# Kernel optimization log

Measured on AMD Instinct MI355X. Metric: run time of the kernel, lower is better.

## Reference

```python
import jax, jax.numpy as jnp
import numpy as np

B, S, D_MODEL = 4, 4096, 2048
D_SPACE = 128
N_C, N_QK, N_V = 512, 512, 512
TOPK_C, TOPK_QK, TOPK_V = 8, 4, 6


def setup_inputs() -> dict:
    key = jax.random.key(0)
    k1, k2, k3, k4 = jax.random.split(key, 4)
    x = jax.random.normal(k1, (B, S, D_MODEL), dtype=jnp.float32)
    importance = jax.random.uniform(k2, (B, S), dtype=jnp.float32)
    proj_w = jax.random.normal(k3, (D_SPACE, D_MODEL), dtype=jnp.float32) * (1.0 / np.sqrt(D_MODEL))
    proj_b = jnp.zeros((D_SPACE,), dtype=jnp.float32)
    neuron_emb = jax.random.normal(k4, (N_C + N_QK + N_V, D_SPACE), dtype=jnp.float32) * 0.02
    return {"x": x, "importance": importance, "proj_w": proj_w, "proj_b": proj_b, "neuron_emb": neuron_emb}


def _topk_sparsify(w, k):
    # torch: topk -> scatter into zeros -> renormalize
    vals, idx = jax.lax.top_k(w, k)                      # [B,k]
    b = jnp.arange(w.shape[0])[:, None]
    sparse = jnp.zeros_like(w).at[b, idx].set(vals)      # [B,n]
    return sparse / (sparse.sum(axis=-1, keepdims=True) + 1e-8)


def reference(x, importance, proj_w, proj_b, neuron_emb):
    # eval mode: dropout off, no starvation bonus, no EMA / aux loss
    h = jnp.einsum("bsd,ed->bse", x, proj_w) + proj_b          # [B,S,d_space]
    nrm = jnp.linalg.norm(neuron_emb, axis=-1, keepdims=True)
    emb_n = neuron_emb / jnp.maximum(nrm, 1e-12)               # F.normalize
    logits = jnp.einsum("bse,ne->bsn", h, emb_n)               # [B,S,total]

    log_c = logits[..., :N_C]
    log_qk = logits[..., N_C:N_C + N_QK]                        # expand_Q == expand_K slice
    log_v = logits[..., N_C + N_QK:]

    pref_c = jax.nn.softmax(log_c, axis=-1)
    pref_qk = jax.nn.softmax(log_qk, axis=-1)
    pref_v = jax.nn.softmax(log_v, axis=-1)

    dense_c = jnp.einsum("bs,bsn->bn", importance, pref_c)
    dense_qk = jnp.einsum("bs,bsn->bn", importance, pref_qk)
    dense_v = jnp.einsum("bs,bsn->bn", importance, pref_v)

    cw = _topk_sparsify(dense_c, TOPK_C)
    qw = _topk_sparsify(dense_qk, TOPK_QK)   # Q and K use identical logits in eval
    kw = _topk_sparsify(dense_qk, TOPK_QK)
    vw = _topk_sparsify(dense_v, TOPK_V)
    return jnp.stack([cw, qw, kw, vw])       # [4, B, 512]
```

## Files before the change

kernel.cpp:

```cpp
#include <hip/hip_runtime.h>
#include <hip/hip_bf16.h>

#define BATCH 4
#define S_TOT 4096
#define ROWS (BATCH * S_TOT)
#define DM 2048
#define DSP 128
#define NSEG 512

typedef short short8 __attribute__((ext_vector_type(8)));
typedef float f32x16 __attribute__((ext_vector_type(16)));

static __device__ inline short f2bf(float v, float& back) {
  unsigned u = __float_as_uint(v);
  unsigned r = u + 0x7FFFu + ((u >> 16) & 1u);
  unsigned short hs = (unsigned short)(r >> 16);
  back = __uint_as_float(((unsigned)hs) << 16);
  return (short)hs;
}

#define GLL16(gsrc, ldst)                                                       \
  __builtin_amdgcn_global_load_lds(                                             \
      (const __attribute__((address_space(1))) void*)(gsrc),                    \
      (__attribute__((address_space(3))) void*)(ldst), 16, 0, 0)


__global__ __launch_bounds__(64) void k0_prep(const float* __restrict__ W,
                                              const float* __restrict__ emb,
                                              short* __restrict__ wHi,
                                              short* __restrict__ wLo,
                                              short* __restrict__ eHi,
                                              short* __restrict__ eLo) {
  const int l = threadIdx.x;
  if (blockIdx.x < 512) {
    const int tc = blockIdx.x;
    const int t = tc >> 7, c = tc & 127;
    const int n = t * 32 + (l & 31);
    const int k = c * 16 + (l >> 5) * 8;
    const float4 a0 = *(const float4*)&W[(size_t)n * DM + k];
    const float4 a1 = *(const float4*)&W[(size_t)n * DM + k + 4];
    const float av[8] = {a0.x, a0.y, a0.z, a0.w, a1.x, a1.y, a1.z, a1.w};
    short8 hi8, lo8; float bk;
    #pragma unroll
    for (int e = 0; e < 8; ++e) {
      hi8[e] = f2bf(av[e], bk); lo8[e] = f2bf(av[e] - bk, bk);
    }
    const size_t idx = (size_t)tc * 64 + l;
    ((short8*)wHi)[idx] = hi8;
    ((short8*)wLo)[idx] = lo8;
  } else {
    const int row = blockIdx.x - 512;
    __shared__ short sh[128], sl[128];
    float2 v = *(const float2*)&emb[row * 128 + l * 2];
    float ss = v.x * v.x + v.y * v.y;
    #pragma unroll
    for (int m = 32; m; m >>= 1) ss += __shfl_xor(ss, m);
    const float inv = 1.0f / fmaxf(sqrtf(ss), 1e-12f);
    float bk;
    const float ox = v.x * inv, oy = v.y * inv;
    sh[2 * l] = f2bf(ox, bk);     sl[2 * l] = f2bf(ox - bk, bk);
    sh[2 * l + 1] = f2bf(oy, bk); sl[2 * l + 1] = f2bf(oy - bk, bk);
    __syncthreads();
    if (l < 32) {
      const int split = l >> 4, kc = (l >> 1) & 7, kh = l & 1;
      const short* src = (split ? sl : sh) + kc * 16 + kh * 8;
      const short8 val = *(const short8*)src;
      const size_t idx = (size_t)(row >> 5) * 4096 + kc * 512 +
                         ((row & 31) + 32 * kh) * 8;
      *(short8*)((split ? eLo : eHi) + idx) = val;
    }
  }
}

__global__ __launch_bounds__(512, 4) void k1_fused(const float* __restrict__ x,
                                                   const short* __restrict__ wHi,
                                                   const short* __restrict__ wLo,
                                                   const float* __restrict__ bias,
                                                   short* __restrict__ hHi,
                                                   short* __restrict__ hLo) {
  __shared__ __align__(16) float As[2][32][128];
  __shared__ __align__(16) float hsum[32][132];
  __shared__ float bsh[128];
  const int t = threadIdx.x;
  const int wave = t >> 6, lane = t & 63;
  const int fr = lane & 31, ks = lane >> 5;
  const int kh = wave >> 2, wc = wave & 3;
  const int m0 = blockIdx.x * 32;

  if (t < 128) bsh[t] = bias[t];

  const int r0 = 4 * wave + ks;
  const int r1 = r0 + 2;
  const float* xsrc0 = x + (size_t)(m0 + r0) * DM + ((fr ^ (r0 & 7)) << 2);
  const float* xsrc1 = x + (size_t)(m0 + r1) * DM + ((fr ^ (r1 & 7)) << 2);
  float* AsF = &As[0][0][0];
  float* dst0 = AsF + wave * 512;
  float* dst1 = dst0 + 256;

  const short8* bhBase = (const short8*)wHi + (size_t)(wc * 128) * 64 + lane;
  const short8* blBase = (const short8*)wLo + (size_t)(wc * 128) * 64 + lane;
  const int fr7 = fr & 7;

  f32x16 acc = {};

  GLL16(xsrc0, dst0);
  GLL16(xsrc1, dst1);
  __syncthreads();

  #pragma unroll 2
  for (int step = 0; step < 16; ++step) {
    const int buf = step & 1;
    if (step + 1 < 16) {
      GLL16(xsrc0 + (step + 1) * 128, AsF + (buf ^ 1) * 4096 + wave * 512);
      GLL16(xsrc1 + (step + 1) * 128, AsF + (buf ^ 1) * 4096 + wave * 512 + 256);
    }
    const float* abase = AsF + buf * 4096 + fr * 128;
    #pragma unroll
    for (int c = 0; c < 4; ++c) {
      const int g0 = kh * 16 + c * 4 + ks * 2;
      const float4 a0 = *(const float4*)(abase + ((g0 ^ fr7) << 2));
      const float4 a1 = *(const float4*)(abase + (((g0 + 1) ^ fr7) << 2));
      const float av[8] = {a0.x, a0.y, a0.z, a0.w, a1.x, a1.y, a1.z, a1.w};
      short8 ah, al; float bk;
      #pragma unroll
      for (int e = 0; e < 8; ++e) {
        ah[e] = f2bf(av[e], bk); al[e] = f2bf(av[e] - bk, bk);
      }
      const int kcg = step * 8 + kh * 4 + c;
      const short8 bh = bhBase[(size_t)kcg * 64];
      const short8 bl = blBase[(size_t)kcg * 64];
      acc = __builtin_amdgcn_mfma_f32_32x32x16_bf16(ah, bh, acc, 0, 0, 0);
      acc = __builtin_amdgcn_mfma_f32_32x32x16_bf16(ah, bl, acc, 0, 0, 0);
      acc = __builtin_amdgcn_mfma_f32_32x32x16_bf16(al, bh, acc, 0, 0, 0);
    }
    __syncthreads();
  }

  if (kh == 0) {
    #pragma unroll
    for (int reg = 0; reg < 16; ++reg) {
      const int row = (reg & 3) + 8 * (reg >> 2) + 4 * ks;
      hsum[row][wc * 32 + fr] = acc[reg];
    }
  }
  __syncthreads();
  if (kh == 1) {
    #pragma unroll
    for (int reg = 0; reg < 16; ++reg) {
      const int row = (reg & 3) + 8 * (reg >> 2) + 4 * ks;
      hsum[row][wc * 32 + fr] += acc[reg];
    }
  }
  __syncthreads();

  {
    const int row = t >> 4, kc8 = t & 15;
    float v[8];
    #pragma unroll
    for (int j = 0; j < 8; ++j)
      v[j] = hsum[row][kc8 * 8 + j] + bsh[kc8 * 8 + j];
    short8 hi8, lo8; float bk;
    #pragma unroll
    for (int e = 0; e < 8; ++e) {
      hi8[e] = f2bf(v[e], bk); lo8[e] = f2bf(v[e] - bk, bk);
    }
    const int kc = kc8 >> 1, kh2 = kc8 & 1;
    const size_t idx = (size_t)blockIdx.x * 512 + kc * 64 + (row + 32 * kh2);
    ((short8*)hHi)[idx] = hi8;
    ((short8*)hLo)[idx] = lo8;
  }
}

__global__ __launch_bounds__(512, 2) void k2_mfma(const short* __restrict__ hHi,
                                                  const short* __restrict__ hLo,
                                                  const short* __restrict__ eHi,
                                                  const short* __restrict__ eLo,
                                                  const float* __restrict__ imp,
                                                  float* __restrict__ partials) {
  const int t = threadIdx.x;
  const int m0 = blockIdx.x * 64;
  const int seg = blockIdx.y;
  const int wave = t >> 6, lane = t & 63;
  const int wr = wave >> 2;
  const int wc = wave & 3;
  const int fr = lane & 31;
  const int hi = lane >> 5;

  __shared__ float redA[2][32][4];
  __shared__ float redB[2][32][4];
  __shared__ float ldsD[2][512];

  f32x16 acc[4] = {};

  const short8* pAh = (const short8*)hHi + ((m0 >> 5) + wr) * 512 + lane;
  const short8* pAl = (const short8*)hLo + ((m0 >> 5) + wr) * 512 + lane;
  const short8* pBh = (const short8*)eHi + (seg * 16 + wc * 4) * 512 + lane;
  const short8* pBl = (const short8*)eLo + (seg * 16 + wc * 4) * 512 + lane;

  #pragma unroll
  for (int kc = 0; kc < 8; ++kc) {
    const short8 ah = pAh[kc * 64];
    const short8 al = pAl[kc * 64];
    #pragma unroll
    for (int t2 = 0; t2 < 4; ++t2) {
      const short8 bh = pBh[t2 * 512 + kc * 64];
      const short8 bl = pBl[t2 * 512 + kc * 64];
      acc[t2] = __builtin_amdgcn_mfma_f32_32x32x16_bf16(ah, bh, acc[t2], 0, 0, 0);
      acc[t2] = __builtin_amdgcn_mfma_f32_32x32x16_bf16(ah, bl, acc[t2], 0, 0, 0);
      acc[t2] = __builtin_amdgcn_mfma_f32_32x32x16_bf16(al, bh, acc[t2], 0, 0, 0);
    }
  }

  float mx[16];
  #pragma unroll
  for (int r = 0; r < 16; ++r) {
    float m = fmaxf(fmaxf(acc[0][r], acc[1][r]), fmaxf(acc[2][r], acc[3][r]));
    #pragma unroll
    for (int k = 1; k < 32; k <<= 1) m = fmaxf(m, __shfl_xor(m, k));
    mx[r] = m;
  }
  if (fr == 0) {
    #pragma unroll
    for (int r = 0; r < 16; ++r)
      redA[wr][(r & 3) + 8 * (r >> 2) + 4 * hi][wc] = mx[r];
  }
  __syncthreads();
  float M[16];
  #pragma unroll
  for (int r = 0; r < 16; ++r) {
    const int row = (r & 3) + 8 * (r >> 2) + 4 * hi;
    M[r] = fmaxf(fmaxf(redA[wr][row][0], redA[wr][row][1]),
                 fmaxf(redA[wr][row][2], redA[wr][row][3]));
  }

  float sm[16];
  #pragma unroll
  for (int r = 0; r < 16; ++r) {
    float s = 0.0f;
    #pragma unroll
    for (int t2 = 0; t2 < 4; ++t2) {
      const float p = __expf(acc[t2][r] - M[r]);
      acc[t2][r] = p;
      s += p;
    }
    #pragma unroll
    for (int k = 1; k < 32; k <<= 1) s += __shfl_xor(s, k);
    sm[r] = s;
  }
  if (fr == 0) {
    #pragma unroll
    for (int r = 0; r < 16; ++r)
      redB[wr][(r & 3) + 8 * (r >> 2) + 4 * hi][wc] = sm[r];
  }
  __syncthreads();
  float w[16];
  #pragma unroll
  for (int r = 0; r < 16; ++r) {
    const int row = (r & 3) + 8 * (r >> 2) + 4 * hi;
    const float S = (redB[wr][row][0] + redB[wr][row][1]) +
                    (redB[wr][row][2] + redB[wr][row][3]);
    w[r] = imp[m0 + wr * 32 + row] / S;
  }

  #pragma unroll
  for (int t2 = 0; t2 < 4; ++t2) {
    float d = 0.0f;
    #pragma unroll
    for (int r = 0; r < 16; ++r) d = fmaf(acc[t2][r], w[r], d);
    d += __shfl_xor(d, 32);
    if (hi == 0) ldsD[wr][wc * 128 + t2 * 32 + fr] = d;
  }
  __syncthreads();
  partials[((size_t)seg * 256 + blockIdx.x) * 512 + t] = ldsD[0][t] + ldsD[1][t];
}

__global__ __launch_bounds__(256) void k3_topk(const float* __restrict__ partials,
                                               float* __restrict__ out) {
  const int b = blockIdx.x;
  const int seg = blockIdx.y;
  const int tid = threadIdx.x;
  const int K = (seg == 0) ? 8 : ((seg == 1) ? 4 : 6);

  __shared__ float v[512];
  __shared__ float wv[8];
  __shared__ int wi[8];
  __shared__ float redv[4];
  __shared__ int redi[4];

  const float* src = partials + ((size_t)seg * 256 + b * 64) * 512;
  float a0 = 0.f, a1 = 0.f, a2 = 0.f, a3 = 0.f;
  float b0 = 0.f, b1 = 0.f, b2 = 0.f, b3 = 0.f;
  for (int j = 0; j < 64; j += 4) {
    a0 += src[(size_t)(j + 0) * 512 + tid];
    a1 += src[(size_t)(j + 1) * 512 + tid];
    a2 += src[(size_t)(j + 2) * 512 + tid];
    a3 += src[(size_t)(j + 3) * 512 + tid];
    b0 += src[(size_t)(j + 0) * 512 + tid + 256];
    b1 += src[(size_t)(j + 1) * 512 + tid + 256];
    b2 += src[(size_t)(j + 2) * 512 + tid + 256];
    b3 += src[(size_t)(j + 3) * 512 + tid + 256];
  }
  v[tid] = (a0 + a1) + (a2 + a3);
  v[tid + 256] = (b0 + b1) + (b2 + b3);
  __syncthreads();

  for (int t = 0; t < K; ++t) {
    const float v0 = v[tid], v1 = v[tid + 256];
    float bv; int bi;
    if (v1 > v0) { bv = v1; bi = tid + 256; } else { bv = v0; bi = tid; }
    #pragma unroll
    for (int m = 1; m < 64; m <<= 1) {
      const float ov = __shfl_xor(bv, m);
      const int oi = __shfl_xor(bi, m);
      if (ov > bv || (ov == bv && oi < bi)) { bv = ov; bi = oi; }
    }
    if ((tid & 63) == 0) { redv[tid >> 6] = bv; redi[tid >> 6] = bi; }
    __syncthreads();
    if (tid == 0) {
      float best = redv[0]; int besti = redi[0];
      for (int q = 1; q < 4; ++q)
        if (redv[q] > best || (redv[q] == best && redi[q] < besti)) {
          best = redv[q]; besti = redi[q];
        }
      wv[t] = best; wi[t] = besti;
      v[besti] = -3.0e38f;
    }
    __syncthreads();
  }

  float s = 1e-8f;
  for (int t = 0; t < K; ++t) s += wv[t];

  const int slot0 = (seg == 0) ? 0 : ((seg == 1) ? 1 : 3);
  float* o0 = out + slot0 * (BATCH * NSEG) + b * NSEG;
  o0[tid] = 0.0f; o0[tid + 256] = 0.0f;
  float* o1 = nullptr;
  if (seg == 1) {
    o1 = out + 2 * (BATCH * NSEG) + b * NSEG;
    o1[tid] = 0.0f; o1[tid + 256] = 0.0f;
  }
  __syncthreads();
  if (tid < K) {
    const float val = wv[tid] / s;
    o0[wi[tid]] = val;
    if (seg == 1) o1[wi[tid]] = val;
  }
}

extern "C" void kernel_launch(void* const* d_in, const int* in_sizes, int n_in,
                              void* d_out, int out_size, void* d_ws, size_t ws_size,
                              hipStream_t stream) {
  (void)in_sizes; (void)n_in; (void)out_size; (void)ws_size;
  const float* x    = (const float*)d_in[0];
  const float* imp  = (const float*)d_in[1];
  const float* W    = (const float*)d_in[2];
  const float* bias = (const float*)d_in[3];
  const float* emb  = (const float*)d_in[4];
  float* out = (float*)d_out;

  float* partials = (float*)d_ws;
  short* hHi      = (short*)(partials + 768 * 512);
  short* hLo      = hHi + 2097152;
  short* eHi      = hLo + 2097152;
  short* eLo      = eHi + 196608;
  short* wHi      = eLo + 196608;
  short* wLo      = wHi + 262144;

  k0_prep<<<512 + 1536, 64, 0, stream>>>(W, emb, wHi, wLo, eHi, eLo);
  k1_fused<<<ROWS / 32, 512, 0, stream>>>(x, wHi, wLo, bias, hHi, hLo);
  k2_mfma<<<dim3(ROWS / 64, 3), 512, 0, stream>>>(hHi, hLo, eHi, eLo, imp, partials);
  k3_topk<<<dim3(BATCH, 3), 256, 0, stream>>>(partials, out);
}
```

Measured before the change: 113.1 us.

## Double k1 row tile to 64, drop split-K reduction, use packed bf16 convert

```diff
diff --git a/kernel.cpp b/kernel.cpp
--- a/kernel.cpp
+++ b/kernel.cpp
@@ -17,6 +17,25 @@
   unsigned short hs = (unsigned short)(r >> 16);
   back = __uint_as_float(((unsigned)hs) << 16);
   return (short)hs;
+}
+
+static __device__ inline unsigned cvtpk2(float a, float b) {
+  unsigned r;
+  asm("v_cvt_pk_bf16_f32 %0, %1, %2" : "=v"(r) : "v"(a), "v"(b));
+  return r;
+}
+static __device__ inline void cvt8(const float* v, short8& hi8, short8& lo8) {
+  union { short8 s; unsigned u[4]; } H, L;
+  #pragma unroll
+  for (int w = 0; w < 4; ++w) {
+    const float f0 = v[2 * w], f1 = v[2 * w + 1];
+    const unsigned u = cvtpk2(f0, f1);
+    const float b0 = __uint_as_float(u << 16);
+    const float b1 = __uint_as_float(u & 0xffff0000u);
+    L.u[w] = cvtpk2(f0 - b0, f1 - b1);
+    H.u[w] = u;
+  }
+  hi8 = H.s; lo8 = L.s;
 }
 
 #define GLL16(gsrc, ldst)                                                       \
@@ -72,100 +91,88 @@
   }
 }
 
-__global__ __launch_bounds__(512, 4) void k1_fused(const float* __restrict__ x,
+__global__ __launch_bounds__(512, 2) void k1_fused(const float* __restrict__ x,
                                                    const short* __restrict__ wHi,
                                                    const short* __restrict__ wLo,
                                                    const float* __restrict__ bias,
                                                    short* __restrict__ hHi,
                                                    short* __restrict__ hLo) {
-  __shared__ __align__(16) float As[2][32][128];
-  __shared__ __align__(16) float hsum[32][132];
+  __shared__ __align__(16) float As[2][64][128];
   __shared__ float bsh[128];
   const int t = threadIdx.x;
   const int wave = t >> 6, lane = t & 63;
   const int fr = lane & 31, ks = lane >> 5;
-  const int kh = wave >> 2, wc = wave & 3;
-  const int m0 = blockIdx.x * 32;
+  const int rg = wave >> 2, wc = wave & 3;
+  const int m0 = blockIdx.x * 64;
 
   if (t < 128) bsh[t] = bias[t];
 
-  const int r0 = 4 * wave + ks;
-  const int r1 = r0 + 2;
-  const float* xsrc0 = x + (size_t)(m0 + r0) * DM + ((fr ^ (r0 & 7)) << 2);
-  const float* xsrc1 = x + (size_t)(m0 + r1) * DM + ((fr ^ (r1 & 7)) << 2);
+  const float* xs[4];
+  #pragma unroll
+  for (int j = 0; j < 4; ++j) {
+    const int r = 8 * wave + 2 * j + ks;
+    xs[j] = x + (size_t)(m0 + r) * DM + ((fr ^ (2 * j + ks)) << 2);
+  }
   float* AsF = &As[0][0][0];
-  float* dst0 = AsF + wave * 512;
-  float* dst1 = dst0 + 256;
-
-  const short8* bhBase = (const short8*)wHi + (size_t)(wc * 128) * 64 + lane;
-  const short8* blBase = (const short8*)wLo + (size_t)(wc * 128) * 64 + lane;
-  const int fr7 = fr & 7;
+
+  const short8* bhB = (const short8*)wHi + (size_t)(wc * 128) * 64 + lane;
+  const short8* blB = (const short8*)wLo + (size_t)(wc * 128) * 64 + lane;
 
   f32x16 acc = {};
 
-  GLL16(xsrc0, dst0);
-  GLL16(xsrc1, dst1);
-  __syncthreads();
-
-  #pragma unroll 2
+  #define STAGE(buf, step)                                                      \
+    _Pragma("unroll")                                                           \
+    for (int j = 0; j < 4; ++j)                                                 \
+      GLL16(xs[j] + (step) * 128, AsF + (buf) * 8192 + (8 * wave + 2 * j) * 128);
+
+  STAGE(0, 0);
+  __syncthreads();
+
+  #pragma unroll 1
   for (int step = 0; step < 16; ++step) {
     const int buf = step & 1;
-    if (step + 1 < 16) {
-      GLL16(xsrc0 + (step + 1) * 128, AsF + (buf ^ 1) * 4096 + wave * 512);
-      GLL16(xsrc1 + (step + 1) * 128, AsF + (buf ^ 1) * 4096 + wave * 512 + 256);
-    }
-    const float* abase = AsF + buf * 4096 + fr * 128;
-    #pragma unroll
-    for (int c = 0; c < 4; ++c) {
-      const int g0 = kh * 16 + c * 4 + ks * 2;
-      const float4 a0 = *(const float4*)(abase + ((g0 ^ fr7) << 2));
-      const float4 a1 = *(const float4*)(abase + (((g0 + 1) ^ fr7) << 2));
+    if (step + 1 < 16) STAGE(buf ^ 1, step + 1);
+    const float* abase = AsF + buf * 8192 + (rg * 32 + fr) * 128;
+    const int s7 = fr & 7;
+    #pragma unroll
+    for (int c = 0; c < 8; ++c) {
+      const int g0 = c * 4 + ks * 2;
+      const float4 a0 = *(const float4*)(abase + ((g0 ^ s7) << 2));
+      const float4 a1 = *(const float4*)(abase + (((g0 + 1) ^ s7) << 2));
       const float av[8] = {a0.x, a0.y, a0.z, a0.w, a1.x, a1.y, a1.z, a1.w};
-      short8 ah, al; float bk;
-      #pragma unroll
-      for (int e = 0; e < 8; ++e) {
-        ah[e] = f2bf(av[e], bk); al[e] = f2bf(av[e] - bk, bk);
-      }
-      const int kcg = step * 8 + kh * 4 + c;
-      const short8 bh = bhBase[(size_t)kcg * 64];
-      const short8 bl = blBase[(size_t)kcg * 64];
+      short8 ah, al;
+      cvt8(av, ah, al);
+      const int kc = step * 8 + c;
+      const short8 bh = bhB[(size_t)kc * 64];
+      const short8 bl = blB[(size_t)kc * 64];
       acc = __builtin_amdgcn_mfma_f32_32x32x16_bf16(ah, bh, acc, 0, 0, 0);
       acc = __builtin_amdgcn_mfma_f32_32x32x16_bf16(ah, bl, acc, 0, 0, 0);
       acc = __builtin_amdgcn_mfma_f32_32x32x16_bf16(al, bh, acc, 0, 0, 0);
     }
     __syncthreads();
   }
-
-  if (kh == 0) {
-    #pragma unroll
-    for (int reg = 0; reg < 16; ++reg) {
-      const int row = (reg & 3) + 8 * (reg >> 2) + 4 * ks;
-      hsum[row][wc * 32 + fr] = acc[reg];
-    }
-  }
-  __syncthreads();
-  if (kh == 1) {
-    #pragma unroll
-    for (int reg = 0; reg < 16; ++reg) {
-      const int row = (reg & 3) + 8 * (reg >> 2) + 4 * ks;
-      hsum[row][wc * 32 + fr] += acc[reg];
-    }
-  }
-  __syncthreads();
-
-  {
-    const int row = t >> 4, kc8 = t & 15;
+  #undef STAGE
+
+  float* hsum = AsF;
+  #pragma unroll
+  for (int reg = 0; reg < 16; ++reg) {
+    const int row = (reg & 3) + 8 * (reg >> 2) + 4 * ks;
+    hsum[(rg * 32 + row) * 132 + wc * 32 + fr] = acc[reg];
+  }
+  __syncthreads();
+  #pragma unroll
+  for (int i = 0; i < 2; ++i) {
+    const int task = t + 512 * i;
+    const int row = task >> 4, kc8 = task & 15;
     float v[8];
     #pragma unroll
     for (int j = 0; j < 8; ++j)
-      v[j] = hsum[row][kc8 * 8 + j] + bsh[kc8 * 8 + j];
-    short8 hi8, lo8; float bk;
-    #pragma unroll
-    for (int e = 0; e < 8; ++e) {
-      hi8[e] = f2bf(v[e], bk); lo8[e] = f2bf(v[e] - bk, bk);
-    }
+      v[j] = hsum[row * 132 + kc8 * 8 + j] + bsh[kc8 * 8 + j];
+    short8 hi8, lo8;
+    cvt8(v, hi8, lo8);
     const int kc = kc8 >> 1, kh2 = kc8 & 1;
-    const size_t idx = (size_t)blockIdx.x * 512 + kc * 64 + (row + 32 * kh2);
+    const size_t idx = ((size_t)blockIdx.x * 2 + (row >> 5)) * 512 + kc * 64 +
+                       ((row & 31) + 32 * kh2);
     ((short8*)hHi)[idx] = hi8;
     ((short8*)hLo)[idx] = lo8;
   }
@@ -367,7 +374,7 @@
   short* wLo      = wHi + 262144;
 
   k0_prep<<<512 + 1536, 64, 0, stream>>>(W, emb, wHi, wLo, eHi, eLo);
-  k1_fused<<<ROWS / 32, 512, 0, stream>>>(x, wHi, wLo, bias, hHi, hLo);
+  k1_fused<<<ROWS / 64, 512, 0, stream>>>(x, wHi, wLo, bias, hHi, hLo);
   k2_mfma<<<dim3(ROWS / 64, 3), 512, 0, stream>>>(hHi, hLo, eHi, eLo, imp, partials);
   k3_topk<<<dim3(BATCH, 3), 256, 0, stream>>>(partials, out);
 }
```

Result: slower. 122.8 us (+8.5%).
